# Performance work log

Measured on AMD Instinct MI355X. Metric: run time of the kernel, lower is better.

The kernel has to match this reference:

```python
import jax, jax.numpy as jnp
import numpy as np

N, E, D = 100000, 1600000, 128


def setup_inputs() -> dict:
    key = jax.random.key(0)
    ks = jax.random.split(key, 8)
    s = 1.0 / np.sqrt(D)
    return {
        "x": jax.random.normal(ks[0], (N, D), dtype=jnp.float32),
        "edge_index": jax.random.randint(ks[1], (2, E), 0, N, dtype=jnp.int64),
        "x_prev": jax.random.normal(ks[2], (N, D), dtype=jnp.float32),
        # GCNConv params: weight [in,out], bias [out]
        "W": jax.random.uniform(ks[3], (D, D), jnp.float32, -s, s),
        "b": jnp.zeros((D,), jnp.float32),
        # GRUCell params (torch layout): [3*H, H] gates ordered (r, z, n)
        "W_ih": jax.random.uniform(ks[4], (3 * D, D), jnp.float32, -s, s),
        "W_hh": jax.random.uniform(ks[5], (3 * D, D), jnp.float32, -s, s),
        "b_ih": jax.random.uniform(ks[6], (3 * D,), jnp.float32, -s, s),
        "b_hh": jax.random.uniform(ks[7], (3 * D,), jnp.float32, -s, s),
    }


def _gcn_conv(x, edge_index, W, b):
    n = x.shape[0]
    loop = jnp.arange(n, dtype=edge_index.dtype)
    src = jnp.concatenate([edge_index[0], loop])  # [E+N]
    dst = jnp.concatenate([edge_index[1], loop])
    # symmetric normalization: deg over destinations (incl. self loops)
    deg = jax.ops.segment_sum(jnp.ones_like(dst, dtype=x.dtype), dst, num_segments=n)
    dinv = jnp.where(deg > 0, jax.lax.rsqrt(deg), 0.0)
    norm = dinv[src] * dinv[dst]  # [E+N]
    xw = x @ W  # [N, out]
    msg = xw[src] * norm[:, None]  # gather + scale
    return jax.ops.segment_sum(msg, dst, num_segments=n) + b


def _gru_cell(inp, h, W_ih, W_hh, b_ih, b_hh):
    gi = inp @ W_ih.T + b_ih  # [N, 3H]
    gh = h @ W_hh.T + b_hh
    i_r, i_z, i_n = jnp.split(gi, 3, axis=-1)
    h_r, h_z, h_n = jnp.split(gh, 3, axis=-1)
    r = jax.nn.sigmoid(i_r + h_r)
    z = jax.nn.sigmoid(i_z + h_z)
    ntil = jnp.tanh(i_n + r * h_n)
    return (1.0 - z) * ntil + z * h


def reference(x, edge_index, x_prev, W, b, W_ih, W_hh, b_ih, b_hh):
    h_cur = _gcn_conv(x, edge_index, W, b)
    return _gru_cell(h_cur, x_prev, W_ih, W_hh, b_ih, b_hh)
```

## Files before the change

kernel.cpp:

```cpp
#include <hip/hip_runtime.h>
#include <hip/hip_bf16.h>
#include <math.h>

#define DIM 128
#define PSHIFT 10
#define PSZ 1024
#define CHUNK 4096

typedef __attribute__((ext_vector_type(8))) short bf16x8;
typedef __attribute__((ext_vector_type(4))) float f32x4;
typedef __attribute__((ext_vector_type(2))) float f32x2;
typedef unsigned short u16;
typedef unsigned char u8;
typedef unsigned int u32;
typedef unsigned long long u64;

__device__ __forceinline__ u16 f2bf(float x) {
    u32 u = __builtin_bit_cast(u32, x);
    u += 0x7fff + ((u >> 16) & 1);
    return (u16)(u >> 16);
}
__device__ __forceinline__ float bf2f(u16 h) {
    return __builtin_bit_cast(float, (u32)h << 16);
}
__device__ __forceinline__ float fsig(float x) {
    return __builtin_amdgcn_rcpf(1.f + __expf(-x));
}
__device__ __forceinline__ float ftanh(float x) {
    return 1.f - 2.f * __builtin_amdgcn_rcpf(__expf(2.f * x) + 1.f);
}
__device__ __forceinline__ u8 f2fp8(float v) {
    int pk = __builtin_amdgcn_cvt_pk_fp8_f32(v, v, 0, false);
    return (u8)(pk & 0xff);
}


__global__ __launch_bounds__(256) void k_prepcount(const int* __restrict__ edst,
                                                   int* __restrict__ pcnt, int E,
                                                   const float* __restrict__ W,
                                                   const float* __restrict__ Wih,
                                                   const float* __restrict__ Whh,
                                                   const float4* __restrict__ xp,
                                                   u16* __restrict__ Wt,
                                                   u16* __restrict__ Wihb,
                                                   u16* __restrict__ Whhb,
                                                   u32* __restrict__ Xpb, int n4) {
    __shared__ int h[128];
    int t = threadIdx.x;
    int gid = blockIdx.x * 256 + t;
    int stride = gridDim.x * 256;
    if (t < 128) h[t] = 0;
    __syncthreads();
    for (int e = gid; e < E; e += stride)
        atomicAdd(&h[edst[e] >> PSHIFT], 1);
    for (int i = gid; i < n4; i += stride) {
        float4 v = xp[i];
        Xpb[i * 2 + 0] = (u32)f2bf(v.x) | ((u32)f2bf(v.y) << 16);
        Xpb[i * 2 + 1] = (u32)f2bf(v.z) | ((u32)f2bf(v.w) << 16);
    }
    if (gid < 128 * 128) {
        int k = gid >> 7, c = gid & 127;
        Wt[c * 128 + k] = f2bf(W[gid]);
    }
    if (gid < 3 * 128 * 128) {
        Wihb[gid] = f2bf(Wih[gid]);
        Whhb[gid] = f2bf(Whh[gid]);
    }
    __syncthreads();
    if (t < 128 && h[t]) atomicAdd(&pcnt[t], h[t]);
}

__global__ __launch_bounds__(256) void k_pscan(const int* __restrict__ pcnt,
                                               int* __restrict__ poff,
                                               int* __restrict__ pfill,
                                               int* __restrict__ rowp,
                                               int P, int N, int E) {
    __shared__ int a[256];
    int t = threadIdx.x;
    int v = (t < P) ? pcnt[t] : 0;
    a[t] = v;
    __syncthreads();
    #pragma unroll
    for (int off = 1; off < 256; off <<= 1) {
        int y = (t >= off) ? a[t - off] : 0;
        __syncthreads();
        a[t] += y;
        __syncthreads();
    }
    int excl = a[t] - v;
    if (t < P) { poff[t] = excl; pfill[t] = excl; }
    if (t == 0) { poff[P] = E; rowp[N] = E; }
}

__global__ __launch_bounds__(256) void k_pscatter(const int* __restrict__ esrc,
                                                  const int* __restrict__ edst,
                                                  int* __restrict__ pfill,
                                                  u32* __restrict__ pbuf, int E) {
    __shared__ int hist[128], sc[128], lofs[128], gbase[128];
    __shared__ u32 sp[CHUNK];
    int t = threadIdx.x;
    int c0 = blockIdx.x * CHUNK;
    int cnt = E - c0; if (cnt > CHUNK) cnt = CHUNK;

    if (t < 128) hist[t] = 0;
    __syncthreads();

    u32 s[16], d[16];
    int p[16], r[16];
    #pragma unroll
    for (int j = 0; j < 16; ++j) {
        int i = j * 256 + t;
        if (i < cnt) {
            s[j] = (u32)esrc[c0 + i];
            d[j] = (u32)edst[c0 + i];
            p[j] = (int)(d[j] >> PSHIFT);
            r[j] = atomicAdd(&hist[p[j]], 1);
        }
    }
    __syncthreads();

    if (t < 128) sc[t] = hist[t];
    __syncthreads();
    #pragma unroll
    for (int off = 1; off < 128; off <<= 1) {
        int y = 0;
        if (t < 128 && t >= off) y = sc[t - off];
        __syncthreads();
        if (t < 128) sc[t] += y;
        __syncthreads();
    }
    if (t < 128) {
        lofs[t] = sc[t] - hist[t];
        if (hist[t] > 0) gbase[t] = atomicAdd(&pfill[t], hist[t]);
    }
    __syncthreads();

    #pragma unroll
    for (int j = 0; j < 16; ++j) {
        int i = j * 256 + t;
        if (i < cnt) {
            int idx = lofs[p[j]] + r[j];
            sp[idx] = (s[j] << PSHIFT) | (d[j] & (PSZ - 1));
        }
    }
    __syncthreads();

    #pragma unroll
    for (int j = 0; j < 16; ++j) {
        int i = j * 256 + t;
        if (i < cnt) {
            int idx = lofs[p[j]] + r[j];
        }
    }
    for (int i = t; i < cnt; i += 256) {
        int lo = 0, hi = 127;
        #pragma unroll
        for (int step = 0; step < 7; ++step) {
            int mid = (lo + hi + 1) >> 1;
            if (lofs[mid] <= i) lo = mid; else hi = mid - 1;
        }
        int pp = lo;
        int gpos = gbase[pp] + (i - lofs[pp]);
        pbuf[gpos] = sp[i];
    }
}

__global__ __launch_bounds__(256) void k_pfill(const u32* __restrict__ pbuf,
                                               const int* __restrict__ poff,
                                               int* __restrict__ rowp,
                                               int* __restrict__ srcs,
                                               float* __restrict__ dinv, int N) {
    __shared__ int cnt[PSZ];
    __shared__ int wsum[4];
    int p = blockIdx.x, t = threadIdx.x;
    int lane = t & 63, wid = t >> 6;
    int nb0 = p << PSHIFT;
    int ncnt = N - nb0; if (ncnt > PSZ) ncnt = PSZ;
    int b0 = poff[p], b1 = poff[p + 1];
    int bc = b1 - b0;

    for (int i = t; i < PSZ; i += 256) cnt[i] = 0;
    __syncthreads();
    for (int i = t; i < bc; i += 256) {
        u32 ld = pbuf[b0 + i] & (PSZ - 1);
        atomicAdd(&cnt[ld], 1);
    }
    __syncthreads();

    int base = t * 4;
    int c[4];
    int ssum = 0;
    #pragma unroll
    for (int j = 0; j < 4; ++j) { c[j] = cnt[base + j]; ssum += c[j]; }
    int incl = ssum;
    #pragma unroll
    for (int off = 1; off < 64; off <<= 1) {
        int y = __shfl_up(incl, off, 64);
        if (lane >= off) incl += y;
    }
    if (lane == 63) wsum[wid] = incl;
    __syncthreads();
    int add = 0;
    for (int w = 0; w < wid; ++w) add += wsum[w];
    int rr = b0 + add + (incl - ssum);
    #pragma unroll
    for (int j = 0; j < 4; ++j) {
        int i = base + j;
        if (i < ncnt) {
            rowp[nb0 + i] = rr;
            dinv[nb0 + i] = rsqrtf((float)(c[j] + 1));
        }
        cnt[i] = rr;
        rr += c[j];
    }
    __syncthreads();

    for (int i = t; i < bc; i += 256) {
        u32 v = pbuf[b0 + i];
        u32 ld = v & (PSZ - 1);
        int pos = atomicAdd(&cnt[ld], 1);
        srcs[pos] = (int)(v >> PSHIFT);
    }
}


__global__ __launch_bounds__(256) void k_gemm1(const float* __restrict__ X,
                                               const u16* __restrict__ Wt,
                                               const float* __restrict__ dinv,
                                               u8* __restrict__ XW8, int n) {
    __shared__ u16 Wlds[128 * 128];
    int t = threadIdx.x, w = t >> 6, l = t & 63;
    int lr = l & 15, q = l >> 4;

    for (int cidx = t; cidx < 2048; cidx += 256) {
        int r = cidx >> 4, kc = cidx & 15;
        int dst = r * 128 + ((kc * 8) ^ ((r & 7) << 3));
        *(bf16x8*)(Wlds + dst) = *(const bf16x8*)(Wt + r * 128 + kc * 8);
    }
    __syncthreads();

    int r0 = blockIdx.x * 128;
    int wrow0 = r0 + w * 32;
    int sw = (lr & 7) << 3;
    int ar0 = wrow0 + lr;      if (ar0 > n - 1) ar0 = n - 1;
    int ar1 = wrow0 + 16 + lr; if (ar1 > n - 1) ar1 = n - 1;
    const float* x0 = X + (size_t)ar0 * DIM;
    const float* x1 = X + (size_t)ar1 * DIM;

    f32x4 acc[2][8];
    #pragma unroll
    for (int s = 0; s < 2; ++s)
        #pragma unroll
        for (int c = 0; c < 8; ++c) acc[s][c] = (f32x4){0.f, 0.f, 0.f, 0.f};

    #pragma unroll
    for (int kb = 0; kb < 4; ++kb) {
        int ko = kb * 32 + q * 8;
        float4 f00 = *(const float4*)(x0 + ko), f01 = *(const float4*)(x0 + ko + 4);
        float4 f10 = *(const float4*)(x1 + ko), f11 = *(const float4*)(x1 + ko + 4);
        bf16x8 a0, a1;
        a0[0] = (short)f2bf(f00.x); a0[1] = (short)f2bf(f00.y);
        a0[2] = (short)f2bf(f00.z); a0[3] = (short)f2bf(f00.w);
        a0[4] = (short)f2bf(f01.x); a0[5] = (short)f2bf(f01.y);
        a0[6] = (short)f2bf(f01.z); a0[7] = (short)f2bf(f01.w);
        a1[0] = (short)f2bf(f10.x); a1[1] = (short)f2bf(f10.y);
        a1[2] = (short)f2bf(f10.z); a1[3] = (short)f2bf(f10.w);
        a1[4] = (short)f2bf(f11.x); a1[5] = (short)f2bf(f11.y);
        a1[6] = (short)f2bf(f11.z); a1[7] = (short)f2bf(f11.w);
        int kw = ko ^ sw;
        #pragma unroll
        for (int ct = 0; ct < 8; ++ct) {
            bf16x8 b = *(const bf16x8*)(Wlds + (ct * 16 + lr) * 128 + kw);
            acc[0][ct] = __builtin_amdgcn_mfma_f32_16x16x32_bf16(a0, b, acc[0][ct], 0, 0, 0);
            acc[1][ct] = __builtin_amdgcn_mfma_f32_16x16x32_bf16(a1, b, acc[1][ct], 0, 0, 0);
        }
    }

    float dv[2][4];
    #pragma unroll
    for (int s = 0; s < 2; ++s)
        #pragma unroll
        for (int i = 0; i < 4; ++i) {
            int row = wrow0 + s * 16 + q * 4 + i; if (row > n - 1) row = n - 1;
            dv[s][i] = dinv[row];
        }
    #pragma unroll
    for (int s = 0; s < 2; ++s)
        #pragma unroll
        for (int ct = 0; ct < 8; ++ct)
            #pragma unroll
            for (int i = 0; i < 4; ++i) {
                int row = wrow0 + s * 16 + q * 4 + i;
                if (row < n)
                    XW8[(size_t)row * DIM + ct * 16 + lr] = f2fp8(acc[s][ct][i] * dv[s][i]);
            }
}


__global__ __launch_bounds__(256) void k_gather(const u8* __restrict__ XW8,
                                                const float* __restrict__ dinv,
                                                const int* __restrict__ row_ptr,
                                                const int* __restrict__ srcs,
                                                const float* __restrict__ bias,
                                                u16* __restrict__ Hcb, int n) {
    int node = blockIdx.x * 4 + (threadIdx.x >> 6);
    if (node >= n) return;
    int lane = threadIdx.x & 63;
    int c = lane * 2;

    u16 sv = *(const u16*)(XW8 + (size_t)node * DIM + c);
    f32x2 sf = __builtin_amdgcn_cvt_pk_f32_fp8((int)(u32)sv, false);
    float accx = sf[0], accy = sf[1];

    int e = row_ptr[node], end = row_ptr[node + 1];
    for (; e + 7 < end; e += 8) {
        int sdx[8]; u16 vv[8];
        #pragma unroll
        for (int j = 0; j < 8; ++j) sdx[j] = srcs[e + j];
        #pragma unroll
        for (int j = 0; j < 8; ++j)
            vv[j] = *(const u16*)(XW8 + (size_t)sdx[j] * DIM + c);
        #pragma unroll
        for (int j = 0; j < 8; ++j) {
            f32x2 f = __builtin_amdgcn_cvt_pk_f32_fp8((int)(u32)vv[j], false);
            accx += f[0];
            accy += f[1];
        }
    }
    for (; e < end; ++e) {
        u16 v = *(const u16*)(XW8 + (size_t)srcs[e] * DIM + c);
        f32x2 f = __builtin_amdgcn_cvt_pk_f32_fp8((int)(u32)v, false);
        accx += f[0];
        accy += f[1];
    }
    float di = dinv[node];
    float ox = accx * di + bias[c];
    float oy = accy * di + bias[c + 1];
    *(u32*)(Hcb + (size_t)node * DIM + c) = (u32)f2bf(ox) | ((u32)f2bf(oy) << 16);
}


__global__ __launch_bounds__(256) void k_gru(const u16* __restrict__ Hcb,
                                             const u16* __restrict__ Xpb,
                                             const u16* __restrict__ Wihb,
                                             const u16* __restrict__ Whhb,
                                             const float* __restrict__ bih,
                                             const float* __restrict__ bhh,
                                             float* __restrict__ Out, int n) {
    __shared__ u16 Wlds[96 * 128];
    int t = threadIdx.x, w = t >> 6, l = t & 63;
    int lr = l & 15, q = l >> 4;

    int nwg = gridDim.x;
    int qq = nwg >> 3, rr8 = nwg & 7;
    int xcd = blockIdx.x & 7, idx = blockIdx.x >> 3;
    int logical = (xcd < rr8 ? xcd * (qq + 1) : rr8 * (qq + 1) + (xcd - rr8) * qq) + idx;
    int cs = logical & 7;
    int rb = logical >> 3;
    int c0 = cs * 16;
    int r0 = rb * 256;

    for (int cidx = t; cidx < 1536; cidx += 256) {
        int r = cidx >> 4, kc = cidx & 15;
        int m = (r >= 48);
        int rr = m ? r - 48 : r;
        int g = rr >> 4, cc = rr & 15;
        const u16* src = (m ? Whhb : Wihb) + (size_t)((g << 7) + c0 + cc) * DIM + kc * 8;
        int dst = r * 128 + ((kc * 8) ^ ((r & 7) << 3));
        *(bf16x8*)(Wlds + dst) = *(const bf16x8*)src;
    }
    __syncthreads();

    int sw = (lr & 7) << 3;
    int j = c0 + lr;
    float br = bih[j],       bz = bih[128 + j], bn = bih[256 + j];
    float cr = bhh[j],       cz = bhh[128 + j], cn = bhh[256 + j];

    #pragma unroll 1
    for (int half = 0; half < 2; ++half) {
        int wrow0 = r0 + half * 128 + w * 32;
        if (wrow0 >= n) break;
        int ar0 = wrow0 + lr;      if (ar0 > n - 1) ar0 = n - 1;
        int ar1 = wrow0 + 16 + lr; if (ar1 > n - 1) ar1 = n - 1;
        const u16* hb0 = Hcb + (size_t)ar0 * DIM;
        const u16* hb1 = Hcb + (size_t)ar1 * DIM;
        const u16* xb0 = Xpb + (size_t)ar0 * DIM;
        const u16* xb1 = Xpb + (size_t)ar1 * DIM;

        f32x4 aI[3][2], aH[3][2];
        #pragma unroll
        for (int g = 0; g < 3; ++g)
            #pragma unroll
            for (int s = 0; s < 2; ++s) {
                aI[g][s] = (f32x4){0.f, 0.f, 0.f, 0.f};
                aH[g][s] = (f32x4){0.f, 0.f, 0.f, 0.f};
            }

        #pragma unroll
        for (int kb = 0; kb < 4; ++kb) {
            int ko = kb * 32 + q * 8;
            bf16x8 hA0 = *(const bf16x8*)(hb0 + ko);
            bf16x8 hA1 = *(const bf16x8*)(hb1 + ko);
            bf16x8 xA0 = *(const bf16x8*)(xb0 + ko);
            bf16x8 xA1 = *(const bf16x8*)(xb1 + ko);
            int kw = ko ^ sw;
            #pragma unroll
            for (int g = 0; g < 3; ++g) {
                int ridx = (g * 16 + lr) * 128 + kw;
                bf16x8 bI = *(const bf16x8*)(Wlds + ridx);
                bf16x8 bH = *(const bf16x8*)(Wlds + ridx + 48 * 128);
                aI[g][0] = __builtin_amdgcn_mfma_f32_16x16x32_bf16(hA0, bI, aI[g][0], 0, 0, 0);
                aI[g][1] = __builtin_amdgcn_mfma_f32_16x16x32_bf16(hA1, bI, aI[g][1], 0, 0, 0);
                aH[g][0] = __builtin_amdgcn_mfma_f32_16x16x32_bf16(xA0, bH, aH[g][0], 0, 0, 0);
                aH[g][1] = __builtin_amdgcn_mfma_f32_16x16x32_bf16(xA1, bH, aH[g][1], 0, 0, 0);
            }
        }

        #pragma unroll
        for (int s = 0; s < 2; ++s)
            #pragma unroll
            for (int i = 0; i < 4; ++i) {
                int row = wrow0 + s * 16 + q * 4 + i;
                if (row >= n) continue;
                float ir = aI[0][s][i] + br;
                float iz = aI[1][s][i] + bz;
                float in_ = aI[2][s][i] + bn;
                float hr = aH[0][s][i] + cr;
                float hz = aH[1][s][i] + cz;
                float hn = aH[2][s][i] + cn;
                float rg = fsig(ir + hr);
                float zc = fsig(-(iz + hz));
                float ng = ftanh(in_ + rg * hn);
                float hp = bf2f((u16)Xpb[(size_t)row * DIM + j]);
                Out[(size_t)row * DIM + j] = fmaf(zc, ng - hp, hp);
            }
    }
}


extern "C" void kernel_launch(void* const* d_in, const int* in_sizes, int n_in,
                              void* d_out, int out_size, void* d_ws, size_t ws_size,
                              hipStream_t stream) {
    const float* x     = (const float*)d_in[0];
    const int*   ei    = (const int*)d_in[1];
    const float* xprev = (const float*)d_in[2];
    const float* W     = (const float*)d_in[3];
    const float* b     = (const float*)d_in[4];
    const float* Wih   = (const float*)d_in[5];
    const float* Whh   = (const float*)d_in[6];
    const float* bih   = (const float*)d_in[7];
    const float* bhh   = (const float*)d_in[8];

    int N = in_sizes[0] / DIM;
    int E = in_sizes[1] / 2;
    int P = (N + PSZ - 1) >> PSHIFT;
    const int* esrc = ei;
    const int* edst = ei + E;

    char* p = (char*)d_ws;
    auto alloc = [&](size_t bytes) {
        char* q = p;
        p += (bytes + 255) & ~(size_t)255;
        return q;
    };
    float* dinv = (float*)alloc((size_t)N * 4);
    int*   rowp = (int*)  alloc((size_t)(N + 1) * 4);
    int*   srcs = (int*)  alloc((size_t)E * 4);
    u16*   Hcb  = (u16*)  alloc((size_t)N * DIM * 2);
    u16*   Xpb  = (u16*)  alloc((size_t)N * DIM * 2);
    size_t xwsz = (size_t)N * DIM;
    size_t pbsz = (size_t)E * 4;
    u8*    XW8  = (u8*)   alloc(xwsz > pbsz ? xwsz : pbsz);
    u16*   Wt   = (u16*)  alloc(128 * 128 * 2);
    u16*   Wihb = (u16*)  alloc(3 * 128 * 128 * 2);
    u16*   Whhb = (u16*)  alloc(3 * 128 * 128 * 2);
    int*   pcnt = (int*)  alloc(128 * 4);
    int*   poff = (int*)  alloc(129 * 4);
    int*   pfil = (int*)  alloc(128 * 4);
    u32*   pbuf = (u32*)XW8;
    float* out  = (float*)d_out;

    hipMemsetAsync(pcnt, 0, 128 * 4, stream);
    int n4 = N * DIM / 4;
    k_prepcount<<<2048, 256, 0, stream>>>(edst, pcnt, E, W, Wih, Whh,
                                          (const float4*)xprev,
                                          Wt, Wihb, Whhb, (u32*)Xpb, n4);
    k_pscan   <<<1, 256, 0, stream>>>(pcnt, poff, pfil, rowp, P, N, E);
    int nch = (E + CHUNK - 1) / CHUNK;
    k_pscatter<<<nch, 256, 0, stream>>>(esrc, edst, pfil, pbuf, E);
    k_pfill   <<<P, 256, 0, stream>>>(pbuf, poff, rowp, srcs, dinv, N);
    int nrb = (N + 127) / 128;
    k_gemm1   <<<nrb, 256, 0, stream>>>(x, Wt, dinv, XW8, N);
    k_gather  <<<(N + 3) / 4, 256, 0, stream>>>(XW8, dinv, rowp, srcs, b, Hcb, N);
    int ngb = (N + 255) / 256;
    k_gru     <<<ngb * 8, 256, 0, stream>>>(Hcb, Xpb, Wihb, Whhb, bih, bhh, out, N);
}
```

Baseline: 270.9 us.

## Scatter partition entries directly, vectorize gather accumulation, double GRU rows per block

The partition scatter kernel no longer stages entries in shared memory with a local prefix scan and binary search. Each edge is now written straight to global memory at its atomically reserved base plus its local rank, which removes the LDS staging, several barriers and the per-element search. In exchange the global writes are less coalesced. The gather kernel now accumulates into a packed float2 vector, and the GRU kernel processes 512 rows per block instead of 256, halving the grid so the shared-memory weight loads are amortized over more rows at the cost of fewer blocks.

New measurement: 272.1 us. About the same (+0.4%).

```diff
diff --git a/kernel.cpp b/kernel.cpp
--- a/kernel.cpp
+++ b/kernel.cpp
@@ -96,8 +96,7 @@
                                                   const int* __restrict__ edst,
                                                   int* __restrict__ pfill,
                                                   u32* __restrict__ pbuf, int E) {
-    __shared__ int hist[128], sc[128], lofs[128], gbase[128];
-    __shared__ u32 sp[CHUNK];
+    __shared__ int hist[128], gbase[128];
     int t = threadIdx.x;
     int c0 = blockIdx.x * CHUNK;
     int cnt = E - c0; if (cnt > CHUNK) cnt = CHUNK;
@@ -119,49 +118,14 @@
     }
     __syncthreads();
 
-    if (t < 128) sc[t] = hist[t];
-    __syncthreads();
-    #pragma unroll
-    for (int off = 1; off < 128; off <<= 1) {
-        int y = 0;
-        if (t < 128 && t >= off) y = sc[t - off];
-        __syncthreads();
-        if (t < 128) sc[t] += y;
-        __syncthreads();
-    }
-    if (t < 128) {
-        lofs[t] = sc[t] - hist[t];
-        if (hist[t] > 0) gbase[t] = atomicAdd(&pfill[t], hist[t]);
-    }
+    if (t < 128 && hist[t] > 0) gbase[t] = atomicAdd(&pfill[t], hist[t]);
     __syncthreads();
 
     #pragma unroll
     for (int j = 0; j < 16; ++j) {
         int i = j * 256 + t;
-        if (i < cnt) {
-            int idx = lofs[p[j]] + r[j];
-            sp[idx] = (s[j] << PSHIFT) | (d[j] & (PSZ - 1));
-        }
-    }
-    __syncthreads();
-
-    #pragma unroll
-    for (int j = 0; j < 16; ++j) {
-        int i = j * 256 + t;
-        if (i < cnt) {
-            int idx = lofs[p[j]] + r[j];
-        }
-    }
-    for (int i = t; i < cnt; i += 256) {
-        int lo = 0, hi = 127;
-        #pragma unroll
-        for (int step = 0; step < 7; ++step) {
-            int mid = (lo + hi + 1) >> 1;
-            if (lofs[mid] <= i) lo = mid; else hi = mid - 1;
-        }
-        int pp = lo;
-        int gpos = gbase[pp] + (i - lofs[pp]);
-        pbuf[gpos] = sp[i];
+        if (i < cnt)
+            pbuf[gbase[p[j]] + r[j]] = (s[j] << PSHIFT) | (d[j] & (PSZ - 1));
     }
 }
 
@@ -309,8 +273,7 @@
     int c = lane * 2;
 
     u16 sv = *(const u16*)(XW8 + (size_t)node * DIM + c);
-    f32x2 sf = __builtin_amdgcn_cvt_pk_f32_fp8((int)(u32)sv, false);
-    float accx = sf[0], accy = sf[1];
+    f32x2 acc = __builtin_amdgcn_cvt_pk_f32_fp8((int)(u32)sv, false);
 
     int e = row_ptr[node], end = row_ptr[node + 1];
     for (; e + 7 < end; e += 8) {
@@ -321,21 +284,16 @@
         for (int j = 0; j < 8; ++j)
             vv[j] = *(const u16*)(XW8 + (size_t)sdx[j] * DIM + c);
         #pragma unroll
-        for (int j = 0; j < 8; ++j) {
-            f32x2 f = __builtin_amdgcn_cvt_pk_f32_fp8((int)(u32)vv[j], false);
-            accx += f[0];
-            accy += f[1];
-        }
+        for (int j = 0; j < 8; ++j)
+            acc += __builtin_amdgcn_cvt_pk_f32_fp8((int)(u32)vv[j], false);
     }
     for (; e < end; ++e) {
         u16 v = *(const u16*)(XW8 + (size_t)srcs[e] * DIM + c);
-        f32x2 f = __builtin_amdgcn_cvt_pk_f32_fp8((int)(u32)v, false);
-        accx += f[0];
-        accy += f[1];
+        acc += __builtin_amdgcn_cvt_pk_f32_fp8((int)(u32)v, false);
     }
     float di = dinv[node];
-    float ox = accx * di + bias[c];
-    float oy = accy * di + bias[c + 1];
+    float ox = acc[0] * di + bias[c];
+    float oy = acc[1] * di + bias[c + 1];
     *(u32*)(Hcb + (size_t)node * DIM + c) = (u32)f2bf(ox) | ((u32)f2bf(oy) << 16);
 }
 
@@ -358,7 +316,7 @@
     int cs = logical & 7;
     int rb = logical >> 3;
     int c0 = cs * 16;
-    int r0 = rb * 256;
+    int r0 = rb * 512;
 
     for (int cidx = t; cidx < 1536; cidx += 256) {
         int r = cidx >> 4, kc = cidx & 15;
@@ -377,7 +335,7 @@
     float cr = bhh[j],       cz = bhh[128 + j], cn = bhh[256 + j];
 
     #pragma unroll 1
-    for (int half = 0; half < 2; ++half) {
+    for (int half = 0; half < 4; ++half) {
         int wrow0 = r0 + half * 128 + w * 32;
         if (wrow0 >= n) break;
         int ar0 = wrow0 + lr;      if (ar0 > n - 1) ar0 = n - 1;
@@ -492,6 +450,6 @@
     int nrb = (N + 127) / 128;
     k_gemm1   <<<nrb, 256, 0, stream>>>(x, Wt, dinv, XW8, N);
     k_gather  <<<(N + 3) / 4, 256, 0, stream>>>(XW8, dinv, rowp, srcs, b, Hcb, N);
-    int ngb = (N + 255) / 256;
+    int ngb = (N + 511) / 512;
     k_gru     <<<ngb * 8, 256, 0, stream>>>(Hcb, Xpb, Wihb, Whhb, bih, bhh, out, N);
 }
```
